# Kernel optimization log

Measured on AMD Instinct MI355X. Metric: run time of the kernel, lower is better.

Reference implementation:

```python
import math
import jax, jax.numpy as jnp
import numpy as np

T, D, H = 2048, 2048, 16
C = D // H
EPS = 1e-6


def _rope_tables(c, t):
    inv_freq = 1.0 / (10000.0 ** (jnp.arange(0, c, 2, dtype=jnp.float32) / c))
    freqs = jnp.arange(t, dtype=jnp.float32)[:, None] * inv_freq[None, :]  # (T, C/2)
    return jnp.sin(freqs), jnp.cos(freqs)


def _rotate_every_two(x):
    x1 = x[..., ::2]
    x2 = x[..., 1::2]
    return jnp.stack((-x2, x1), axis=-1).reshape(x.shape)


def _apply_rope(x_htc, sin, cos):
    # sin/cos: (T, C/2) -> repeat each freq twice along channel -> (1, T, C)
    sin = jnp.repeat(sin, 2, axis=-1)[None]
    cos = jnp.repeat(cos, 2, axis=-1)[None]
    return x_htc * cos + _rotate_every_two(x_htc) * sin


def _layernorm(x, w):
    mu = jnp.mean(x, axis=-1, keepdims=True)
    var = jnp.var(x, axis=-1, keepdims=True)
    return (x - mu) / jnp.sqrt(var + EPS) * w


def setup_inputs() -> dict:
    key = jax.random.key(0)
    ks = jax.random.split(key, 4)
    x = jax.random.normal(ks[0], (T, D), dtype=jnp.float32)
    W_attn = jax.random.normal(ks[1], (3 * D, D), dtype=jnp.float32) * 0.02
    b_attn = jnp.zeros((3 * D,), dtype=jnp.float32)
    W_proj = jax.random.normal(ks[2], (D, D), dtype=jnp.float32) * 0.02
    b_proj = jnp.zeros((D,), dtype=jnp.float32)
    q_ln_w = jnp.ones((C,), dtype=jnp.float32)
    k_ln_w = jnp.ones((C,), dtype=jnp.float32)
    return {"x": x, "W_attn": W_attn, "b_attn": b_attn, "W_proj": W_proj,
            "b_proj": b_proj, "q_ln_w": q_ln_w, "k_ln_w": k_ln_w}


def reference(x, W_attn, b_attn, W_proj, b_proj, q_ln_w, k_ln_w):
    t, d = x.shape
    qkv = x @ W_attn.T + b_attn                      # (T, 3D)
    q, k, v = jnp.split(qkv, 3, axis=-1)
    q = q.reshape(t, H, C).transpose(1, 0, 2)        # (H, T, C)
    k = k.reshape(t, H, C).transpose(1, 0, 2)
    v = v.reshape(t, H, C).transpose(1, 0, 2)
    q = _layernorm(q, q_ln_w)
    k = _layernorm(k, k_ln_w)
    sin, cos = _rope_tables(C, t)
    q = _apply_rope(q, sin, cos)
    k = _apply_rope(k, sin, cos)
    a = jnp.einsum("htc,hsc->hts", q, k)             # (H, T, T)
    causal = jnp.tril(jnp.ones((1, t, t))) == 0
    a = jnp.where(causal, float("-inf"), a)
    scaling = math.sqrt(C)                            # q_ln active
    a = jax.nn.softmax(a.astype(jnp.float32) / scaling, axis=-1).astype(x.dtype)
    out = jnp.einsum("hts,hsc->htc", a, v)           # (H, T, C)
    out = out.transpose(1, 0, 2).reshape(t, d)       # (T, D)
    return out @ W_proj.T + b_proj
```

## Files before the change

kernel.cpp:

```cpp
#include <hip/hip_runtime.h>
#include <hip/hip_bf16.h>
#include <math.h>

#define T_DIM 2048
#define D_DIM 2048
#define H_DIM 16
#define C_DIM 128

typedef __bf16 bf16;
typedef __attribute__((ext_vector_type(8))) __bf16 bf16x8;
typedef __attribute__((ext_vector_type(4))) __bf16 bf16x4;
typedef __attribute__((ext_vector_type(2))) __bf16 bf16x2;
typedef __attribute__((ext_vector_type(4))) float f32x4;

__device__ __forceinline__ void gload_lds16(const void* g, void* l) {
  __builtin_amdgcn_global_load_lds((__attribute__((address_space(1))) void*)g,
                                   (__attribute__((address_space(3))) void*)l,
                                   16, 0, 0);
}

__global__ __launch_bounds__(256) void cvt_f32_to_bf16(
    const float* __restrict__ src, bf16* __restrict__ dst, int n4)
{
  int i = blockIdx.x * blockDim.x + threadIdx.x;
  int stride = gridDim.x * blockDim.x;
  for (; i < n4; i += stride) {
    float4 v = reinterpret_cast<const float4*>(src)[i];
    bf16x4 o;
    o[0] = (bf16)v.x; o[1] = (bf16)v.y; o[2] = (bf16)v.z; o[3] = (bf16)v.w;
    reinterpret_cast<bf16x4*>(dst)[i] = o;
  }
}

__global__ __launch_bounds__(256) void gemm_bt_bias(
    const bf16* __restrict__ A, const bf16* __restrict__ B,
    const float* __restrict__ bias, float* __restrict__ C,
    int M, int N, int K)
{
  __shared__ __align__(16) bf16 As[128 * 32];
  __shared__ __align__(16) bf16 Bs[128 * 32];
  const int tid = threadIdx.x;
  const int lane = tid & 63;
  const int w = tid >> 6;
  const int wm = (w >> 1) * 64, wn = (w & 1) * 64;
  const int g = lane >> 4;
  const int r16 = lane & 15;
  const int bm = blockIdx.y, bn = blockIdx.x;

  f32x4 acc[4][4] = {};

  const size_t Abase = (size_t)(bm * 128) * K;
  const size_t Bbase = (size_t)(bn * 128) * K;

  for (int k0 = 0; k0 < K; k0 += 32) {
#pragma unroll
    for (int c = 0; c < 2; ++c) {
      int e = c * 256 + tid;
      int row = e >> 2, col = (e & 3) * 8;
      gload_lds16(A + Abase + (size_t)row * K + k0 + col, (char*)As + (size_t)e * 16);
      gload_lds16(B + Bbase + (size_t)row * K + k0 + col, (char*)Bs + (size_t)e * 16);
    }
    __syncthreads();
    bf16x8 a[4], b[4];
#pragma unroll
    for (int m = 0; m < 4; ++m)
      a[m] = *reinterpret_cast<const bf16x8*>(&As[(wm + m * 16 + r16) * 32 + g * 8]);
#pragma unroll
    for (int n = 0; n < 4; ++n)
      b[n] = *reinterpret_cast<const bf16x8*>(&Bs[(wn + n * 16 + r16) * 32 + g * 8]);
#pragma unroll
    for (int m = 0; m < 4; ++m)
#pragma unroll
      for (int n = 0; n < 4; ++n)
        acc[m][n] = __builtin_amdgcn_mfma_f32_16x16x32_bf16(a[m], b[n], acc[m][n], 0, 0, 0);
    __syncthreads();
  }

#pragma unroll
  for (int m = 0; m < 4; ++m) {
    int row0 = bm * 128 + wm + m * 16 + g * 4;
#pragma unroll
    for (int n = 0; n < 4; ++n) {
      int col = bn * 128 + wn + n * 16 + r16;
      float bv = bias[col];
#pragma unroll
      for (int rr = 0; rr < 4; ++rr)
        C[(size_t)(row0 + rr) * N + col] = acc[m][n][rr] + bv;
    }
  }
}

__global__ __launch_bounds__(256) void ln_rope_kernel(
    const float* __restrict__ qkv, const float* __restrict__ qw,
    const float* __restrict__ kw, bf16* __restrict__ qo, bf16* __restrict__ ko)
{
  const int tid = threadIdx.x;
  const int lane = tid & 63;
  const int wid = blockIdx.x * 4 + (tid >> 6);
  const int h = wid >> 11;
  const int t = wid & (T_DIM - 1);
  const int c0 = lane * 2;

  float inv_freq = exp2f(-13.287712379549449f * (float)c0 * (1.0f / 128.0f));
  float fr = (float)t * inv_freq;
  float sn = sinf(fr), cs = cosf(fr);
  const float scaleq = 0.08838834764831845f;

#pragma unroll
  for (int which = 0; which < 2; ++which) {
    const float* base = qkv + (size_t)t * (3 * D_DIM) + which * D_DIM + h * C_DIM;
    float2 v = *reinterpret_cast<const float2*>(base + c0);
    float s = v.x + v.y;
#pragma unroll
    for (int m = 32; m; m >>= 1) s += __shfl_xor(s, m);
    float mu = s * (1.0f / 128.0f);
    float d0 = v.x - mu, d1 = v.y - mu;
    float ss = d0 * d0 + d1 * d1;
#pragma unroll
    for (int m = 32; m; m >>= 1) ss += __shfl_xor(ss, m);
    float rstd = rsqrtf(ss * (1.0f / 128.0f) + 1e-6f);
    const float* wgt = which ? kw : qw;
    float x0 = d0 * rstd * wgt[c0], x1 = d1 * rstd * wgt[c0 + 1];
    float o0 = x0 * cs - x1 * sn;
    float o1 = x1 * cs + x0 * sn;
    if (!which) { o0 *= scaleq; o1 *= scaleq; }
    bf16* out = (which ? ko : qo) + ((size_t)h * T_DIM + t) * C_DIM + c0;
    bf16x2 ob; ob[0] = (bf16)o0; ob[1] = (bf16)o1;
    *reinterpret_cast<bf16x2*>(out) = ob;
  }
}

__global__ __launch_bounds__(256) void v_transpose_kernel(
    const float* __restrict__ qkv, bf16* __restrict__ vt)
{
  __shared__ bf16 tile[32][33];
  const int h = blockIdx.z;
  const int t0 = blockIdx.x * 32, c0 = blockIdx.y * 32;
  const int tx = threadIdx.x, ty = threadIdx.y;
#pragma unroll
  for (int i = 0; i < 4; ++i) {
    int t = t0 + ty + i * 8;
    tile[ty + i * 8][tx] =
        (bf16)qkv[(size_t)t * (3 * D_DIM) + 2 * D_DIM + h * C_DIM + c0 + tx];
  }
  __syncthreads();
#pragma unroll
  for (int i = 0; i < 4; ++i) {
    int c = c0 + ty + i * 8;
    vt[((size_t)h * C_DIM + c) * T_DIM + t0 + tx] = tile[tx][ty + i * 8];
  }
}

__global__ __launch_bounds__(256, 4) void attn_kernel(
    const bf16* __restrict__ Q, const bf16* __restrict__ K,
    const bf16* __restrict__ VT, bf16* __restrict__ AO,
    float* __restrict__ U, float* __restrict__ ML)
{
  __shared__ __align__(16) bf16 Ks[2][32 * 128];
  __shared__ __align__(16) bf16 Vs[2][128 * 32];
  __shared__ __align__(16) bf16 p_lds[4][16 * 32];
  const int tid = threadIdx.x;
  const int lane = tid & 63;
  const int w = tid >> 6;
  const int g = lane >> 4, r16 = lane & 15;
  const int h = blockIdx.y;
  const int b = blockIdx.x;

  int qb, kb0, kb1, sp;
  if (b < 32) { qb = 16 + (b >> 1); sp = b & 1; kb0 = sp * 32; kb1 = sp ? (2 * qb + 2) : 32; }
  else        { qb = 47 - b;        sp = -1;    kb0 = 0;       kb1 = 2 * qb + 2; }
  const int qr0 = qb * 64 + w * 16;
  const int qrow = qr0 + r16;

  const bf16* Qh = Q + (size_t)h * T_DIM * C_DIM;
  const bf16* Kh = K + (size_t)h * T_DIM * C_DIM;
  const bf16* Vh = VT + (size_t)h * C_DIM * T_DIM;

  bf16x8 qf[4];
#pragma unroll
  for (int kk = 0; kk < 4; ++kk)
    qf[kk] = *reinterpret_cast<const bf16x8*>(
        &Qh[(size_t)qrow * C_DIM + kk * 32 + g * 8]);

  float mrow = -INFINITY, lrow = 0.f;
  f32x4 o[8] = {};

  auto stage = [&](int bb, int kb) {
    const bf16* Kt = Kh + (size_t)(kb * 32) * C_DIM;
    const bf16* Vt = Vh + kb * 32;
#pragma unroll
    for (int i = 0; i < 2; ++i) {
      int e = i * 256 + tid;
      int r = e >> 4, p = e & 15, j = p ^ (r & 7);
      gload_lds16(Kt + r * C_DIM + j * 8, (char*)&Ks[bb][0] + (size_t)e * 16);
    }
#pragma unroll
    for (int i = 0; i < 2; ++i) {
      int e = i * 256 + tid;
      int r = e >> 2, p = e & 3, j = p ^ ((r >> 1) & 3);
      gload_lds16(Vt + (size_t)r * T_DIM + j * 8, (char*)&Vs[bb][0] + (size_t)e * 16);
    }
  };

  stage(0, kb0);
  __syncthreads();
  int buf = 0;

  for (int kb = kb0; kb < kb1; ++kb) {
    if (kb + 1 < kb1) stage(buf ^ 1, kb + 1);

    f32x4 sacc[2] = {};
    __builtin_amdgcn_s_setprio(1);
#pragma unroll
    for (int n = 0; n < 2; ++n) {
      int kr = n * 16 + r16;
      const bf16* kbase = &Ks[buf][kr << 7];
#pragma unroll
      for (int kk = 0; kk < 4; ++kk) {
        bf16x8 kf = *reinterpret_cast<const bf16x8*>(
            kbase + (((kk * 4 + g) ^ (kr & 7)) << 3));
        sacc[n] = __builtin_amdgcn_mfma_f32_16x16x32_bf16(kf, qf[kk], sacc[n], 0, 0, 0);
      }
    }
    __builtin_amdgcn_s_setprio(0);
    if (kb * 32 + 31 > qr0) {
#pragma unroll
      for (int n = 0; n < 2; ++n)
#pragma unroll
        for (int rr = 0; rr < 4; ++rr)
          if (kb * 32 + n * 16 + g * 4 + rr > qrow) sacc[n][rr] = -3.0e38f;
    }
    float mx = fmaxf(fmaxf(fmaxf(sacc[0][0], sacc[0][1]), fmaxf(sacc[0][2], sacc[0][3])),
                     fmaxf(fmaxf(sacc[1][0], sacc[1][1]), fmaxf(sacc[1][2], sacc[1][3])));
    mx = fmaxf(mx, __shfl_xor(mx, 16));
    mx = fmaxf(mx, __shfl_xor(mx, 32));
    float alpha = 1.0f;
    bool need = __any(mx > mrow + 8.0f);
    if (need) {
      float mnew = fmaxf(mrow, mx);
      alpha = __expf(mrow - mnew);
      mrow = mnew;
    }
    float ps = 0.f;
#pragma unroll
    for (int n = 0; n < 2; ++n)
#pragma unroll
      for (int rr = 0; rr < 4; ++rr) {
        float p = __expf(sacc[n][rr] - mrow);
        sacc[n][rr] = p;
        ps += p;
      }
    ps += __shfl_xor(ps, 16);
    ps += __shfl_xor(ps, 32);
    lrow = lrow * alpha + ps;
    if (need) {
#pragma unroll
      for (int nc = 0; nc < 8; ++nc)
#pragma unroll
        for (int rr = 0; rr < 4; ++rr)
          o[nc][rr] *= alpha;
    }
    {
      bf16* prow = &p_lds[w][r16 << 5];
      const int ssw = (r16 >> 1) & 3;
#pragma unroll
      for (int n = 0; n < 2; ++n) {
        bf16x4 pk;
        pk[0] = (bf16)sacc[n][0]; pk[1] = (bf16)sacc[n][1];
        pk[2] = (bf16)sacc[n][2]; pk[3] = (bf16)sacc[n][3];
        int c8 = 2 * n + (g >> 1);
        *reinterpret_cast<bf16x4*>(prow + (((c8 ^ ssw) << 3) | ((g & 1) << 2))) = pk;
      }
    }
    asm volatile("s_waitcnt lgkmcnt(0)" ::: "memory");
    __builtin_amdgcn_s_setprio(1);
    bf16x8 pf = *reinterpret_cast<const bf16x8*>(
        &p_lds[w][(r16 << 5) + ((g ^ ((r16 >> 1) & 3)) << 3)]);
#pragma unroll
    for (int nc = 0; nc < 8; ++nc) {
      int vr = nc * 16 + r16;
      bf16x8 vf = *reinterpret_cast<const bf16x8*>(
          &Vs[buf][(vr << 5) + ((g ^ ((vr >> 1) & 3)) << 3)]);
      o[nc] = __builtin_amdgcn_mfma_f32_16x16x32_bf16(vf, pf, o[nc], 0, 0, 0);
    }
    __builtin_amdgcn_s_setprio(0);
    __syncthreads();
    buf ^= 1;
  }

  if (sp < 0) {
    float inv = 1.0f / lrow;
    bf16* arow = &AO[(size_t)qrow * D_DIM + h * C_DIM + (g << 2)];
#pragma unroll
    for (int nc = 0; nc < 8; ++nc) {
      bf16x4 ob;
      ob[0] = (bf16)(o[nc][0] * inv); ob[1] = (bf16)(o[nc][1] * inv);
      ob[2] = (bf16)(o[nc][2] * inv); ob[3] = (bf16)(o[nc][3] * inv);
      *reinterpret_cast<bf16x4*>(arow + nc * 16) = ob;
    }
  } else {
    const int qi = qb - 16;
    const size_t ubase = ((size_t)(h * 16 + qi) * 2 + sp) * (64 * 128);
    const size_t mlbase = (size_t)(h * 16 + qi) * 256 + sp * 128;
    const int row = w * 16 + r16;
    float* urow = &U[ubase + (size_t)row * 128 + (g << 2)];
#pragma unroll
    for (int nc = 0; nc < 8; ++nc)
      *reinterpret_cast<f32x4*>(urow + nc * 16) = o[nc];
    if (g == 0) {
      ML[mlbase + row] = mrow;
      ML[mlbase + 64 + row] = lrow;
    }
  }
}

__global__ __launch_bounds__(256) void attn_combine(
    const float* __restrict__ U, const float* __restrict__ ML, bf16* __restrict__ AO)
{
  int idx = blockIdx.x * 256 + threadIdx.x;
  int c4 = (idx & 31) * 4;
  int r = idx >> 5;
  int trow = r & 63;
  int qi = (r >> 6) & 15;
  int h = r >> 10;

  size_t mlbase = (size_t)(h * 16 + qi) * 256;
  float m0 = ML[mlbase + trow],       l0 = ML[mlbase + 64 + trow];
  float m1 = ML[mlbase + 128 + trow], l1 = ML[mlbase + 192 + trow];
  float m = fmaxf(m0, m1);
  float a0 = __expf(m0 - m), a1 = __expf(m1 - m);
  float inv = 1.0f / (l0 * a0 + l1 * a1);

  size_t t0 = ((size_t)(h * 16 + qi) * 2) * (64 * 128) + (size_t)trow * 128 + c4;
  float4 u0 = *reinterpret_cast<const float4*>(U + t0);
  float4 u1 = *reinterpret_cast<const float4*>(U + t0 + 64 * 128);
  int t = 1024 + qi * 64 + trow;
  bf16x4 ob;
  ob[0] = (bf16)((u0.x * a0 + u1.x * a1) * inv);
  ob[1] = (bf16)((u0.y * a0 + u1.y * a1) * inv);
  ob[2] = (bf16)((u0.z * a0 + u1.z * a1) * inv);
  ob[3] = (bf16)((u0.w * a0 + u1.w * a1) * inv);
  *reinterpret_cast<bf16x4*>(&AO[(size_t)t * D_DIM + h * C_DIM + c4]) = ob;
}

extern "C" void kernel_launch(void* const* d_in, const int* in_sizes, int n_in,
                              void* d_out, int out_size, void* d_ws, size_t ws_size,
                              hipStream_t stream)
{
  const float* x      = (const float*)d_in[0];
  const float* W_attn = (const float*)d_in[1];
  const float* b_attn = (const float*)d_in[2];
  const float* W_proj = (const float*)d_in[3];
  const float* b_proj = (const float*)d_in[4];
  const float* q_ln_w = (const float*)d_in[5];
  const float* k_ln_w = (const float*)d_in[6];

  char* ws = (char*)d_ws;
  bf16*  x_bf  = (bf16*)(ws + 0);
  bf16*  wa_bf = (bf16*)(ws + 8388608);
  bf16*  wp_bf = (bf16*)(ws + 33554432);
  float* qkv   = (float*)(ws + 41943040);
  bf16*  q_bf  = (bf16*)(ws + 92274688);
  bf16*  k_bf  = (bf16*)(ws + 100663296);
  bf16*  vt    = (bf16*)(ws + 109051904);
  bf16*  ao    = (bf16*)(ws + 117440512);
  float* U  = (float*)(ws + 41943040);
  float* ML = (float*)(ws + 58720256);

  cvt_f32_to_bf16<<<2048, 256, 0, stream>>>(x,      x_bf,  T_DIM * D_DIM / 4);
  cvt_f32_to_bf16<<<2048, 256, 0, stream>>>(W_attn, wa_bf, 3 * D_DIM * D_DIM / 4);
  cvt_f32_to_bf16<<<2048, 256, 0, stream>>>(W_proj, wp_bf, D_DIM * D_DIM / 4);

  gemm_bt_bias<<<dim3(3 * D_DIM / 128, T_DIM / 128), 256, 0, stream>>>(
      x_bf, wa_bf, b_attn, qkv, T_DIM, 3 * D_DIM, D_DIM);

  ln_rope_kernel<<<(H_DIM * T_DIM) / 4, 256, 0, stream>>>(qkv, q_ln_w, k_ln_w, q_bf, k_bf);
  v_transpose_kernel<<<dim3(T_DIM / 32, C_DIM / 32, H_DIM), dim3(32, 8), 0, stream>>>(qkv, vt);

  attn_kernel<<<dim3(48, H_DIM), 256, 0, stream>>>(q_bf, k_bf, vt, ao, U, ML);
  attn_combine<<<2048, 256, 0, stream>>>(U, ML, ao);

  gemm_bt_bias<<<dim3(D_DIM / 128, T_DIM / 128), 256, 0, stream>>>(
      ao, wp_bf, b_proj, (float*)d_out, T_DIM, D_DIM, D_DIM);
}
```

Measured before the change: 208.7 us.

## Add 256x256 pipelined swizzled-LDS GEMM for QKV and double-buffer the projection GEMM

Adds a 512-thread GEMM kernel with 256x256 output tiles and a K-step of 64. It double-buffers LDS through direct global-to-LDS loads, XOR-swizzles the LDS layout, remaps block IDs, and interleaves quadrant MFMA work with prefetch behind raised wave priority. The QKV projection now uses this kernel, aiming for more data reuse and latency hiding than the old 128x128 tile. The original 128x128 GEMM, still used for the output projection, also gains double buffering and priority hints. The risks are that only 192 blocks launch, which can leave CUs idle, and that the heavy LDS use (128KB per block) limits occupancy to one block per CU.

```diff
diff --git a/kernel.cpp b/kernel.cpp
--- a/kernel.cpp
+++ b/kernel.cpp
@@ -32,13 +32,143 @@
   }
 }
 
+__global__ __launch_bounds__(512, 2) void gemm256_bt_bias(
+    const bf16* __restrict__ A, const bf16* __restrict__ B,
+    const float* __restrict__ bias, float* __restrict__ C,
+    int M, int N, int K)
+{
+  __shared__ __align__(16) bf16 Asl[2][256 * 64];
+  __shared__ __align__(16) bf16 Bsl[2][256 * 64];
+  const int tid = threadIdx.x;
+  const int lane = tid & 63;
+  const int wv = tid >> 6;
+  const int g = lane >> 4, r16 = lane & 15;
+
+  int bid = blockIdx.x;
+  int bid2 = (bid & 7) * (gridDim.x >> 3) + (bid >> 3);
+  const int ntn = N >> 8;
+  const int bn = bid2 % ntn, bm = bid2 / ntn;
+
+  const size_t Abase = (size_t)(bm * 256) * K;
+  const size_t Bbase = (size_t)(bn * 256) * K;
+
+  f32x4 acc[2][2][2][4] = {};
+  bf16x8 a[2][2], b[4][2];
+
+  auto stageA = [&](int bb, int ha, int t) {
+#pragma unroll
+    for (int i = 0; i < 2; ++i) {
+      int c = i * 512 + tid;
+      int r = c >> 3, p = c & 7, j = p ^ (r & 7);
+      gload_lds16(A + Abase + (size_t)(ha * 128 + r) * K + t * 64 + j * 8,
+                  (char*)&Asl[bb][0] + ha * 16384 + (size_t)c * 16);
+    }
+  };
+  auto stageB = [&](int bb, int hb, int t) {
+#pragma unroll
+    for (int i = 0; i < 2; ++i) {
+      int c = i * 512 + tid;
+      int r = c >> 3, p = c & 7, j = p ^ (r & 7);
+      gload_lds16(B + Bbase + (size_t)(hb * 128 + r) * K + t * 64 + j * 8,
+                  (char*)&Bsl[bb][0] + hb * 16384 + (size_t)c * 16);
+    }
+  };
+  auto readA = [&](int bufi, int QR) {
+#pragma unroll
+    for (int R = 0; R < 2; ++R) {
+      int ar = QR * 128 + (wv >> 1) * 32 + R * 16 + r16;
+#pragma unroll
+      for (int ks = 0; ks < 2; ++ks)
+        a[R][ks] = *reinterpret_cast<const bf16x8*>(
+            &Asl[bufi][ar * 64 + (((ks * 4 + g) ^ (ar & 7)) << 3)]);
+    }
+  };
+  auto readB = [&](int bufi, int QC) {
+#pragma unroll
+    for (int F = 0; F < 4; ++F) {
+      int br = QC * 128 + (wv & 1) * 64 + F * 16 + r16;
+#pragma unroll
+      for (int ks = 0; ks < 2; ++ks)
+        b[F][ks] = *reinterpret_cast<const bf16x8*>(
+            &Bsl[bufi][br * 64 + (((ks * 4 + g) ^ (br & 7)) << 3)]);
+    }
+  };
+  auto mfma16 = [&](f32x4 (&c2)[2][4]) {
+    __builtin_amdgcn_s_setprio(1);
+#pragma unroll
+    for (int ks = 0; ks < 2; ++ks)
+#pragma unroll
+      for (int R = 0; R < 2; ++R)
+#pragma unroll
+        for (int F = 0; F < 4; ++F)
+          c2[R][F] = __builtin_amdgcn_mfma_f32_16x16x32_bf16(a[R][ks], b[F][ks], c2[R][F], 0, 0, 0);
+    __builtin_amdgcn_s_setprio(0);
+  };
+
+#define MIDSYNC(VM)                                               \
+  asm volatile("s_waitcnt vmcnt(" #VM ")" ::: "memory");          \
+  __builtin_amdgcn_s_barrier();                                   \
+  asm volatile("s_waitcnt lgkmcnt(0)" ::: "memory");              \
+  __builtin_amdgcn_sched_barrier(0);
+
+  stageA(0, 0, 0); stageB(0, 0, 0); stageB(0, 1, 0); stageA(0, 1, 0);
+  asm volatile("s_waitcnt vmcnt(4)" ::: "memory");
+  __builtin_amdgcn_s_barrier();
+
+  const int NT = K >> 6;
+  for (int t = 0; t < NT; ++t) {
+    const int cb = t & 1, nb = cb ^ 1;
+    const bool pf = (t + 1 < NT);
+    readA(cb, 0);
+    readB(cb, 0);
+    if (pf) stageA(nb, 0, t + 1);
+    MIDSYNC(4)
+    mfma16(acc[0][0]);
+    __builtin_amdgcn_s_barrier();
+    readB(cb, 1);
+    if (pf) stageB(nb, 0, t + 1);
+    MIDSYNC(4)
+    mfma16(acc[0][1]);
+    __builtin_amdgcn_s_barrier();
+    readA(cb, 1);
+    if (pf) stageB(nb, 1, t + 1);
+    __builtin_amdgcn_s_barrier();
+    asm volatile("s_waitcnt lgkmcnt(0)" ::: "memory");
+    __builtin_amdgcn_sched_barrier(0);
+    mfma16(acc[1][1]);
+    __builtin_amdgcn_s_barrier();
+    readB(cb, 0);
+    if (pf) stageA(nb, 1, t + 1);
+    MIDSYNC(4)
+    mfma16(acc[1][0]);
+    __builtin_amdgcn_s_barrier();
+  }
+#undef MIDSYNC
+
+#pragma unroll
+  for (int qr = 0; qr < 2; ++qr)
+#pragma unroll
+    for (int qc = 0; qc < 2; ++qc)
+#pragma unroll
+      for (int R = 0; R < 2; ++R)
+#pragma unroll
+        for (int F = 0; F < 4; ++F) {
+          int row0 = bm * 256 + qr * 128 + (wv >> 1) * 32 + R * 16 + g * 4;
+          int col  = bn * 256 + qc * 128 + (wv & 1) * 64 + F * 16 + r16;
+          float bv = bias[col];
+#pragma unroll
+          for (int rr = 0; rr < 4; ++rr)
+            C[(size_t)(row0 + rr) * N + col] = acc[qr][qc][R][F][rr] + bv;
+        }
+}
+
 __global__ __launch_bounds__(256) void gemm_bt_bias(
     const bf16* __restrict__ A, const bf16* __restrict__ B,
     const float* __restrict__ bias, float* __restrict__ C,
     int M, int N, int K)
 {
-  __shared__ __align__(16) bf16 As[128 * 32];
-  __shared__ __align__(16) bf16 Bs[128 * 32];
+  __shared__ __align__(16) bf16 As[2][128 * 32];
+  __shared__ __align__(16) bf16 Bs[2][128 * 32];
   const int tid = threadIdx.x;
   const int lane = tid & 63;
   const int w = tid >> 6;
@@ -52,27 +182,36 @@
   const size_t Abase = (size_t)(bm * 128) * K;
   const size_t Bbase = (size_t)(bn * 128) * K;
 
-  for (int k0 = 0; k0 < K; k0 += 32) {
+  auto stage = [&](int bb, int k0) {
 #pragma unroll
     for (int c = 0; c < 2; ++c) {
       int e = c * 256 + tid;
       int row = e >> 2, col = (e & 3) * 8;
-      gload_lds16(A + Abase + (size_t)row * K + k0 + col, (char*)As + (size_t)e * 16);
-      gload_lds16(B + Bbase + (size_t)row * K + k0 + col, (char*)Bs + (size_t)e * 16);
-    }
-    __syncthreads();
+      gload_lds16(A + Abase + (size_t)row * K + k0 + col, (char*)&As[bb][0] + (size_t)e * 16);
+      gload_lds16(B + Bbase + (size_t)row * K + k0 + col, (char*)&Bs[bb][0] + (size_t)e * 16);
+    }
+  };
+
+  stage(0, 0);
+  __syncthreads();
+
+  for (int k0 = 0; k0 < K; k0 += 32) {
+    const int cur = (k0 >> 5) & 1;
+    if (k0 + 32 < K) stage(cur ^ 1, k0 + 32);
     bf16x8 a[4], b[4];
 #pragma unroll
     for (int m = 0; m < 4; ++m)
-      a[m] = *reinterpret_cast<const bf16x8*>(&As[(wm + m * 16 + r16) * 32 + g * 8]);
+      a[m] = *reinterpret_cast<const bf16x8*>(&As[cur][(wm + m * 16 + r16) * 32 + g * 8]);
 #pragma unroll
     for (int n = 0; n < 4; ++n)
-      b[n] = *reinterpret_cast<const bf16x8*>(&Bs[(wn + n * 16 + r16) * 32 + g * 8]);
+      b[n] = *reinterpret_cast<const bf16x8*>(&Bs[cur][(wn + n * 16 + r16) * 32 + g * 8]);
+    __builtin_amdgcn_s_setprio(1);
 #pragma unroll
     for (int m = 0; m < 4; ++m)
 #pragma unroll
       for (int n = 0; n < 4; ++n)
         acc[m][n] = __builtin_amdgcn_mfma_f32_16x16x32_bf16(a[m], b[n], acc[m][n], 0, 0, 0);
+    __builtin_amdgcn_s_setprio(0);
     __syncthreads();
   }
 
@@ -371,7 +510,7 @@
   cvt_f32_to_bf16<<<2048, 256, 0, stream>>>(W_attn, wa_bf, 3 * D_DIM * D_DIM / 4);
   cvt_f32_to_bf16<<<2048, 256, 0, stream>>>(W_proj, wp_bf, D_DIM * D_DIM / 4);
 
-  gemm_bt_bias<<<dim3(3 * D_DIM / 128, T_DIM / 128), 256, 0, stream>>>(
+  gemm256_bt_bias<<<dim3((T_DIM / 256) * (3 * D_DIM / 256)), dim3(512), 0, stream>>>(
       x_bf, wa_bf, b_attn, qkv, T_DIM, 3 * D_DIM, D_DIM);
 
   ln_rope_kernel<<<(H_DIM * T_DIM) / 4, 256, 0, stream>>>(qkv, q_ln_w, k_ln_w, q_bf, k_bf);
```

Result: faster. 202.2 us (-3.1%).
